# Optimization experiments

Hardware: AMD Instinct MI355X
Metric: run time of the kernel (lower is better)

The kernel has to match this reference:

```python
import jax, jax.numpy as jnp
import numpy as np

N_TOKENS = 2048
HIDDEN = 2880
N_HEADS = 64          # total query heads
N_KV = 8              # key/value heads
Q_MULT = N_HEADS // N_KV
HEAD_DIM = 64
SLIDING_WINDOW = 128  # layer_idx=0 -> sliding-window layer
SM_SCALE = 1.0 / np.sqrt(HEAD_DIM)
RMS_EPS = 1e-5
ROPE_BASE = 150000.0
ROPE_SCALING = 32.0
INIT_CTX = 4096
NTK_ALPHA = 1.0
NTK_BETA = 32.0


def _rope_tables(num_tokens):
    # YaRN NTK-by-parts inverse frequencies (static constants)
    freq = ROPE_BASE ** (np.arange(0, HEAD_DIM, 2, dtype=np.float64) / HEAD_DIM)
    concentration = 0.1 * np.log(ROPE_SCALING) + 1.0
    d_half = HEAD_DIM / 2
    low = d_half * np.log(INIT_CTX / (NTK_BETA * 2 * np.pi)) / np.log(ROPE_BASE)
    high = d_half * np.log(INIT_CTX / (NTK_ALPHA * 2 * np.pi)) / np.log(ROPE_BASE)
    interpolation = 1.0 / (ROPE_SCALING * freq)
    extrapolation = 1.0 / freq
    ramp = (np.arange(d_half) - low) / (high - low)
    m = 1.0 - np.clip(ramp, 0.0, 1.0)
    inv_freq = interpolation * (1.0 - m) + extrapolation * m
    t = np.arange(num_tokens, dtype=np.float64)
    freqs = np.outer(t, inv_freq)
    cos = jnp.asarray((np.cos(freqs) * concentration), dtype=jnp.float32)
    sin = jnp.asarray((np.sin(freqs) * concentration), dtype=jnp.float32)
    return cos, sin  # [num_tokens, HEAD_DIM//2]


def _apply_rotary(x, cos, sin):
    # x: [n, heads, HEAD_DIM]
    c = cos[:, None, :].astype(x.dtype)
    s = sin[:, None, :].astype(x.dtype)
    x1, x2 = jnp.split(x, 2, axis=-1)
    return jnp.concatenate([x1 * c - x2 * s, x2 * c + x1 * s], axis=-1)


def setup_inputs() -> dict:
    key = jax.random.key(0)
    ks = jax.random.split(key, 7)
    return {
        "x": jax.random.normal(ks[0], (N_TOKENS, HIDDEN), jnp.float32),
        "scale": jax.random.uniform(ks[1], (HIDDEN,), jnp.float32, 0.5, 1.5),
        "sink": jax.random.normal(ks[2], (N_HEADS,), jnp.float32),
        "w_qkv": jax.random.normal(ks[3], (HIDDEN, (N_HEADS + 2 * N_KV) * HEAD_DIM), jnp.float32) * 0.02,
        "b_qkv": jax.random.normal(ks[4], ((N_HEADS + 2 * N_KV) * HEAD_DIM,), jnp.float32) * 0.02,
        "w_o": jax.random.normal(ks[5], (N_HEADS * HEAD_DIM, HIDDEN), jnp.float32) * 0.02,
        "b_o": jax.random.normal(ks[6], (HIDDEN,), jnp.float32) * 0.02,
    }


def reference(x, scale, sink, w_qkv, b_qkv, w_o, b_o):
    n = x.shape[0]
    # RMSNorm (fp32)
    t = x.astype(jnp.float32)
    rms = jnp.sqrt(jnp.mean(t * t, axis=-1, keepdims=True) + RMS_EPS)
    t = (t / rms) * scale

    # QKV projection + split
    qkv = t @ w_qkv + b_qkv
    q_sz = N_HEADS * HEAD_DIM
    kv_sz = N_KV * HEAD_DIM
    q = qkv[:, :q_sz].reshape(n, N_HEADS, HEAD_DIM)
    k = qkv[:, q_sz:q_sz + kv_sz].reshape(n, N_KV, HEAD_DIM)
    v = qkv[:, q_sz + kv_sz:].reshape(n, N_KV, HEAD_DIM)

    # RoPE (YaRN)
    cos, sin = _rope_tables(n)
    q = _apply_rotary(q, cos, sin)
    k = _apply_rotary(k, cos, sin)

    # GQA layout: [n, N_KV, Q_MULT, HEAD_DIM]
    qg = q.reshape(n, N_KV, Q_MULT, HEAD_DIM)

    # scores: [N_KV, Q_MULT, n_q, n_kv]
    scores = jnp.einsum('nhgd,mhd->hgnm', qg, k) * SM_SCALE

    # causal + sliding-window mask
    q_pos = jnp.arange(n)[:, None]
    kv_pos = jnp.arange(n)[None, :]
    mask = jnp.where(kv_pos > q_pos, -jnp.inf, 0.0)
    mask = mask + jnp.where((SLIDING_WINDOW > 0) & (q_pos - kv_pos > SLIDING_WINDOW), -jnp.inf, 0.0)
    scores = scores + mask[None, None, :, :].astype(scores.dtype)

    # sink logit appended as extra softmax column, then dropped
    s_col = jnp.broadcast_to(sink.reshape(N_KV, Q_MULT, 1, 1), (N_KV, Q_MULT, n, 1))
    w = jax.nn.softmax(jnp.concatenate([scores, s_col], axis=-1), axis=-1)[..., :-1]

    attn = jnp.einsum('hgnm,mhd->nhgd', w, v).reshape(n, N_HEADS * HEAD_DIM)
    out = attn @ w_o + b_o
    return x + out


if __name__ == '__main__':
    inp = setup_inputs()
    y = reference(**inp)
    print(y.shape, y.dtype)
```

## Files before the change

### kernel.cpp

```cpp
#include <hip/hip_runtime.h>
#include <cstdint>
#include <cstddef>

#define HIDDEN   2880
#define QKV_N    5120
#define OPROJ_K  4096
#define NTOK     2048
#define WIN      128
#define SM_SCALE 0.125f

typedef _Float16 half8  __attribute__((ext_vector_type(8)));
typedef _Float16 half4v __attribute__((ext_vector_type(4)));
typedef float    f32x4  __attribute__((ext_vector_type(4)));

__device__ __forceinline__ void gload16(const void* g, void* l) {
  __builtin_amdgcn_global_load_lds((__attribute__((address_space(1))) void*)g,
                                   (__attribute__((address_space(3))) void*)l,
                                   16, 0, 0);
}

__device__ __forceinline__ _Float16 f2h(float f) { return (_Float16)f; }

#define NB_T0  (80 * 45)
#define NB_T1  (46 * 64)
#define NB_ROPE 256

__device__ __forceinline__ void cast_transpose64(const float* __restrict__ W,
                                                 _Float16* __restrict__ Wt,
                                                 int K, int N, int n0, int k0,
                                                 float* tile ) {
  int t = threadIdx.x;
  #pragma unroll
  for (int p = 0; p < 16; ++p) {
    int r = p * 4 + (t >> 6), cc = t & 63;
    float vv = 0.f;
    if (n0 + cc < N) vv = W[(size_t)(k0 + r) * N + n0 + cc];
    tile[r * 65 + cc] = vv;
  }
  __syncthreads();
  #pragma unroll
  for (int p = 0; p < 2; ++p) {
    int idx = p * 256 + t;
    int r = idx >> 3, ch = (idx & 7) * 8;
    half8 h;
    #pragma unroll
    for (int u = 0; u < 8; ++u) h[u] = (_Float16)tile[(ch + u) * 65 + r];
    *(half8*)&Wt[(size_t)(n0 + r) * K + k0 + ch] = h;
  }
}

__global__ __launch_bounds__(256) void prep_kernel(const float* __restrict__ x,
                                                   const float* __restrict__ scale,
                                                   const float* __restrict__ w_qkv,
                                                   const float* __restrict__ w_o,
                                                   _Float16* __restrict__ a_h,
                                                   _Float16* __restrict__ wtq,
                                                   _Float16* __restrict__ wto,
                                                   float2* __restrict__ tab) {
  __shared__ float smem[64 * 65];
  int b = blockIdx.x, t = threadIdx.x;
  if (b < NB_T0) {
    cast_transpose64(w_qkv, wtq, HIDDEN, QKV_N, (b % 80) * 64, (b / 80) * 64, smem);
    return;
  }
  b -= NB_T0;
  if (b < NB_T1) {
    cast_transpose64(w_o, wto, OPROJ_K, HIDDEN, (b % 46) * 64, (b / 46) * 64, smem);
    return;
  }
  b -= NB_T1;
  if (b < NTOK) {
    int row = b;
    const float4* xr = (const float4*)(x + (size_t)row * HIDDEN);
    const float4* sc = (const float4*)scale;
    float4 v0 = xr[t];
    float4 v1 = xr[t + 256];
    float4 v2 = (t < 208) ? xr[t + 512] : make_float4(0.f, 0.f, 0.f, 0.f);
    float ss = v0.x*v0.x + v0.y*v0.y + v0.z*v0.z + v0.w*v0.w
             + v1.x*v1.x + v1.y*v1.y + v1.z*v1.z + v1.w*v1.w
             + v2.x*v2.x + v2.y*v2.y + v2.z*v2.z + v2.w*v2.w;
    #pragma unroll
    for (int m = 1; m < 64; m <<= 1) ss += __shfl_xor(ss, m, 64);
    if ((t & 63) == 0) smem[t >> 6] = ss;
    __syncthreads();
    float inv = 1.0f / sqrtf((smem[0] + smem[1] + smem[2] + smem[3]) * (1.0f / HIDDEN) + 1e-5f);
    _Float16* orow = a_h + (size_t)row * HIDDEN;
    auto store4 = [&](int c4, const float4& v, const float4& s) {
      half4v h;
      h[0] = f2h(v.x * inv * s.x); h[1] = f2h(v.y * inv * s.y);
      h[2] = f2h(v.z * inv * s.z); h[3] = f2h(v.w * inv * s.w);
      *(half4v*)(orow + (size_t)c4 * 4) = h;
    };
    store4(t, v0, sc[t]);
    store4(t + 256, v1, sc[t + 256]);
    if (t < 208) store4(t + 512, v2, sc[t + 512]);
    return;
  }
  b -= NTOK;
  {
    int idx = b * 256 + t;
    int tok = idx >> 5, d = idx & 31;
    const double PI = 3.14159265358979323846;
    double i = (double)d;
    double lf = log(150000.0);
    double freq = exp(lf * (i / 32.0));
    double interp = 1.0 / (32.0 * freq);
    double extrap = 1.0 / freq;
    double low  = 32.0 * log(4096.0 / (32.0 * 2.0 * PI)) / lf;
    double high = 32.0 * log(4096.0 / (2.0 * PI)) / lf;
    double ramp = (i - low) / (high - low);
    double mm = 1.0 - fmin(fmax(ramp, 0.0), 1.0);
    double invf = interp * (1.0 - mm) + extrap * mm;
    double ang = (double)tok * invf;
    double conc = 0.1 * log(32.0) + 1.0;
    tab[idx] = make_float2((float)(cos(ang) * conc), (float)(sin(ang) * conc));
  }
}

#define QBM 128
#define QBN 320

__global__ __launch_bounds__(512, 2) void qkv8_kernel(const _Float16* __restrict__ A,
                                                      const _Float16* __restrict__ Bt,
                                                      const float* __restrict__ bias,
                                                      const float2* __restrict__ tab,
                                                      _Float16* __restrict__ out,
                                                      int K) {
  extern __shared__ char smem[];
  int tid = threadIdx.x;
  int wave = tid >> 6, lane = tid & 63;
  int wm = wave >> 2, wn = wave & 3;
  int c = lane & 15, quad = lane >> 4;
  int n0 = blockIdx.x * QBN, m0 = blockIdx.y * QBM;
  int NT = K >> 6;

  const _Float16* gA[2];
  #pragma unroll
  for (int i = 0; i < 2; ++i) {
    int ci = i * 512 + tid, r = ci >> 3, lc = (ci & 7) ^ (r & 7);
    gA[i] = A + (size_t)(m0 + r) * K + lc * 8;
  }
  const _Float16* gB[5];
  #pragma unroll
  for (int i = 0; i < 5; ++i) {
    int ci = i * 512 + tid, r = ci >> 3, lc = (ci & 7) ^ (r & 7);
    gB[i] = Bt + (size_t)(n0 + r) * K + lc * 8;
  }
  char* lA = smem + (size_t)(wave * 64) * 16;
  char* lB = smem + 32768 + (size_t)(wave * 64) * 16;

  auto STAGE = [&](int sel, int t) {
    size_t ko = (size_t)t * 64;
    #pragma unroll
    for (int i = 0; i < 2; ++i) gload16(gA[i] + ko, lA + sel * 16384 + i * 8192);
    #pragma unroll
    for (int i = 0; i < 5; ++i) gload16(gB[i] + ko, lB + sel * 40960 + i * 8192);
  };

  int aoff[2], boff[2];
  #pragma unroll
  for (int ks = 0; ks < 2; ++ks) {
    int px = ((ks * 4 + quad) ^ (c & 7)) * 16;
    aoff[ks] = (wm * 64 + c) * 128 + px;
    boff[ks] = (wn * 80 + c) * 128 + px;
  }

  f32x4 acc[4][5] = {};
  STAGE(0, 0);
  STAGE(1, 1);

  #pragma unroll 1
  for (int t = 0; t < NT; ++t) {
    if (t + 1 < NT) asm volatile("s_waitcnt vmcnt(7)" ::: "memory");
    else            asm volatile("s_waitcnt vmcnt(0)" ::: "memory");
    __builtin_amdgcn_s_barrier();
    asm volatile("" ::: "memory");
    const char* Ab = smem + (t & 1) * 16384;
    const char* Bb = smem + 32768 + (t & 1) * 40960;
    half8 a[4][2], b[5][2];
    #pragma unroll
    for (int i = 0; i < 4; ++i) {
      a[i][0] = *(const half8*)(Ab + aoff[0] + i * 2048);
      a[i][1] = *(const half8*)(Ab + aoff[1] + i * 2048);
    }
    #pragma unroll
    for (int j = 0; j < 5; ++j) {
      b[j][0] = *(const half8*)(Bb + boff[0] + j * 2048);
      b[j][1] = *(const half8*)(Bb + boff[1] + j * 2048);
    }
    __builtin_amdgcn_s_setprio(1);
    #pragma unroll
    for (int j = 0; j < 5; ++j)
      #pragma unroll
      for (int i = 0; i < 4; ++i)
        acc[i][j] = __builtin_amdgcn_mfma_f32_16x16x32_f16(a[i][0], b[j][0], acc[i][j], 0, 0, 0);
    __builtin_amdgcn_s_setprio(0);
    asm volatile("s_waitcnt lgkmcnt(0)" ::: "memory");
    __builtin_amdgcn_s_barrier();
    asm volatile("" ::: "memory");
    if (t + 2 < NT) STAGE(t & 1, t + 2);
    __builtin_amdgcn_s_setprio(1);
    #pragma unroll
    for (int j = 0; j < 5; ++j)
      #pragma unroll
      for (int i = 0; i < 4; ++i)
        acc[i][j] = __builtin_amdgcn_mfma_f32_16x16x32_f16(a[i][1], b[j][1], acc[i][j], 0, 0, 0);
    __builtin_amdgcn_s_setprio(0);
  }

  asm volatile("s_waitcnt lgkmcnt(0)" ::: "memory");
  __builtin_amdgcn_s_barrier();
  asm volatile("" ::: "memory");
  float* fP = (float*)smem;
  #pragma unroll
  for (int h = 0; h < 2; ++h) {
    if (wm == h) {
      #pragma unroll
      for (int j = 0; j < 5; ++j) {
        int coll = wn * 80 + j * 16 + c;
        float bv = bias[n0 + coll];
        #pragma unroll
        for (int i = 0; i < 4; ++i) {
          int rowl = i * 16 + quad * 4;
          #pragma unroll
          for (int r = 0; r < 4; ++r)
            fP[(rowl + r) * 324 + coll] = acc[i][j][r] + bv;
        }
      }
    }
    asm volatile("s_waitcnt lgkmcnt(0)" ::: "memory");
    __builtin_amdgcn_s_barrier();
    asm volatile("" ::: "memory");
    #pragma unroll
    for (int p = 0; p < 20; ++p) {
      int idx = p * 512 + tid;
      int row = idx / 160, s = idx - row * 160;
      int head = s >> 5, d = s & 31;
      int coll = head * 64 + d;
      int gcol = n0 + coll;
      int grow = m0 + h * 64 + row;
      float x1 = fP[row * 324 + coll];
      float x2 = fP[row * 324 + coll + 32];
      float2 cs = (gcol < 4608) ? tab[(size_t)grow * 32 + d] : make_float2(1.f, 0.f);
      out[(size_t)grow * QKV_N + gcol]      = f2h(x1 * cs.x - x2 * cs.y);
      out[(size_t)grow * QKV_N + gcol + 32] = f2h(x2 * cs.x + x1 * cs.y);
    }
    if (h == 0) {
      asm volatile("s_waitcnt lgkmcnt(0)" ::: "memory");
      __builtin_amdgcn_s_barrier();
      asm volatile("" ::: "memory");
    }
  }
}

template <int BM, bool QKV_MODE, int MINW>
__global__ __launch_bounds__(256, MINW) void gemm_kernel(const _Float16* __restrict__ A,
                                                         const _Float16* __restrict__ Bt,
                                                         const float* __restrict__ bias,
                                                         const float* __restrict__ resid,
                                                         const float2* __restrict__ tab,
                                                         void* __restrict__ Cout,
                                                         int M, int N, int K) {
  constexpr int MI = BM / 32;
  constexpr int NA = BM / 32;
  __shared__ _Float16 Alds[BM * 64];
  __shared__ _Float16 Blds[128 * 64];
  int tid = threadIdx.x;
  int wave = tid >> 6, lane = tid & 63;
  int wm = wave >> 1, wn = wave & 1;
  int c = lane & 15, quad = lane >> 4;
  int m0 = blockIdx.y * BM, n0 = blockIdx.x * 128;

  const _Float16* gAp[NA]; _Float16* lAp[NA];
  #pragma unroll
  for (int i = 0; i < NA; ++i) {
    int p = wave * 64 + i * 256 + lane;
    int r = p >> 3;
    int kl = (p & 7) ^ (r & 7);
    gAp[i] = A + (size_t)(m0 + r) * K + kl * 8;
    lAp[i] = Alds + (size_t)(wave * 64 + i * 256) * 8;
  }
  const _Float16* gBp[4]; _Float16* lBp[4];
  #pragma unroll
  for (int i = 0; i < 4; ++i) {
    int p = wave * 64 + i * 256 + lane;
    int r = p >> 3;
    int kl = (p & 7) ^ (r & 7);
    gBp[i] = Bt + (size_t)(n0 + r) * K + kl * 8;
    lBp[i] = Blds + (size_t)(wave * 64 + i * 256) * 8;
  }

  int px[2];
  px[0] = ((0 * 4 + quad) ^ (c & 7)) * 8;
  px[1] = ((1 * 4 + quad) ^ (c & 7)) * 8;

  f32x4 acc[MI][4] = {};
  int nIter = K >> 6;
  for (int kt = 0; kt < nIter; ++kt) {
    __syncthreads();
    #pragma unroll
    for (int i = 0; i < NA; ++i) { gload16(gAp[i], lAp[i]); gAp[i] += 64; }
    #pragma unroll
    for (int i = 0; i < 4; ++i)  { gload16(gBp[i], lBp[i]); gBp[i] += 64; }
    __syncthreads();
    half8 a[MI][2], b[4][2];
    #pragma unroll
    for (int i = 0; i < MI; ++i) {
      int row = wm * (BM / 2) + i * 16 + c;
      a[i][0] = *(const half8*)&Alds[row * 64 + px[0]];
      a[i][1] = *(const half8*)&Alds[row * 64 + px[1]];
    }
    #pragma unroll
    for (int j = 0; j < 4; ++j) {
      int row = wn * 64 + j * 16 + c;
      b[j][0] = *(const half8*)&Blds[row * 64 + px[0]];
      b[j][1] = *(const half8*)&Blds[row * 64 + px[1]];
    }
    #pragma unroll
    for (int i = 0; i < MI; ++i)
      #pragma unroll
      for (int j = 0; j < 4; ++j) {
        acc[i][j] = __builtin_amdgcn_mfma_f32_16x16x32_f16(a[i][0], b[j][0], acc[i][j], 0, 0, 0);
        acc[i][j] = __builtin_amdgcn_mfma_f32_16x16x32_f16(a[i][1], b[j][1], acc[i][j], 0, 0, 0);
      }
  }

  if (QKV_MODE) {
    _Float16* outp = (_Float16*)Cout;
    bool ropeTile = (n0 < 4608);
    #pragma unroll
    for (int i = 0; i < MI; ++i) {
      int rowb = m0 + wm * (BM / 2) + i * 16 + quad * 4;
      if (ropeTile) {
        #pragma unroll
        for (int jp = 0; jp < 2; ++jp) {
          int col = n0 + wn * 64 + jp * 16 + c;
          float b1 = bias[col], b2 = bias[col + 32];
          #pragma unroll
          for (int r = 0; r < 4; ++r) {
            float2 cs = tab[(size_t)(rowb + r) * 32 + jp * 16 + c];
            float x1 = acc[i][jp][r] + b1;
            float x2 = acc[i][jp + 2][r] + b2;
            outp[(size_t)(rowb + r) * QKV_N + col]      = f2h(x1 * cs.x - x2 * cs.y);
            outp[(size_t)(rowb + r) * QKV_N + col + 32] = f2h(x2 * cs.x + x1 * cs.y);
          }
        }
      } else {
        #pragma unroll
        for (int j = 0; j < 4; ++j) {
          int col = n0 + wn * 64 + j * 16 + c;
          float bv = bias[col];
          #pragma unroll
          for (int r = 0; r < 4; ++r)
            outp[(size_t)(rowb + r) * QKV_N + col] = f2h(acc[i][j][r] + bv);
        }
      }
    }
  } else {
    float* outp = (float*)Cout;
    #pragma unroll
    for (int i = 0; i < MI; ++i) {
      int rowb = m0 + wm * (BM / 2) + i * 16 + quad * 4;
      #pragma unroll
      for (int j = 0; j < 4; ++j) {
        int col = n0 + wn * 64 + j * 16 + c;
        if (col < N) {
          float bv = bias[col];
          #pragma unroll
          for (int r = 0; r < 4; ++r)
            outp[(size_t)(rowb + r) * N + col] =
                acc[i][j][r] + bv + resid[(size_t)(rowb + r) * N + col];
        }
      }
    }
  }
}

#define TQ 16
__global__ __launch_bounds__(256) void attn_kernel(const _Float16* __restrict__ qkv,
                                                   const float* __restrict__ sink,
                                                   _Float16* __restrict__ attn_out) {
  __shared__ __align__(16) char smem[61440];
  _Float16* Klds = (_Float16*)smem;
  _Float16* Qlds = (_Float16*)(smem + 20480);
  _Float16* Ps   = (_Float16*)smem;
  _Float16* Vt   = (_Float16*)(smem + 40960);

  int qt = blockIdx.x, kvh = blockIdx.y;
  int Q0 = qt * TQ;
  int kmin = (Q0 >= WIN) ? Q0 - WIN : 0;
  int nkv = Q0 + TQ - kmin;
  int tid = threadIdx.x;
  int wave = tid >> 6, lane = tid & 63;
  int c = lane & 15, quad = lane >> 4;

  {
    const _Float16* kbase = qkv + 4096 + kvh * 64;
    #pragma unroll
    for (int p = 0; p < 5; ++p) {
      int ci = p * 256 + wave * 64 + lane;
      int row = ci >> 3, pc = ci & 7;
      int lc = pc ^ (row & 7);
      gload16(kbase + (size_t)(kmin + row) * QKV_N + lc * 8,
              (char*)Klds + (size_t)(p * 256 + wave * 64) * 16);
    }
  }
  {
    const _Float16* qbase = qkv + kvh * 512;
    #pragma unroll
    for (int p = 0; p < 4; ++p) {
      int ci = p * 256 + wave * 64 + lane;
      int tok = ci >> 6, Lp = ci & 63;
      int Llog = (Lp & 56) | ((Lp ^ tok) & 7);
      gload16(qbase + (size_t)(Q0 + tok) * QKV_N + Llog * 8,
              (char*)Qlds + (size_t)(p * 256 + wave * 64) * 16);
    }
  }
  #pragma unroll
  for (int p = 0; p < 5; ++p) {
    int cc = p * 256 + tid;
    int col = cc % 160;
    int d0 = (cc / 160) * 8;
    union { uint4 u4; _Float16 hv[8]; } buf;
    if (col < nkv) buf.u4 = *(const uint4*)(qkv + (size_t)(kmin + col) * QKV_N + 4608 + kvh * 64 + d0);
    else           buf.u4 = make_uint4(0, 0, 0, 0);
    #pragma unroll
    for (int uu = 0; uu < 8; ++uu) Vt[(d0 + uu) * 160 + col] = buf.hv[uu];
  }

  __syncthreads();

  half8 aq[2][2];
  #pragma unroll
  for (int i = 0; i < 2; ++i) {
    int qm = wave * 2 + i;
    #pragma unroll
    for (int ks = 0; ks < 2; ++ks) {
      int kc = ks * 4 + quad;
      int Lp = qm * 8 + (kc ^ (c & 7));
      aq[i][ks] = *(const half8*)&Qlds[c * 512 + Lp * 8];
    }
  }

  f32x4 sacc[2][9] = {};
  #pragma unroll
  for (int j = 0; j < 9; ++j) {
    #pragma unroll
    for (int ks = 0; ks < 2; ++ks) {
      int kc = ks * 4 + quad;
      int pc = kc ^ (c & 7);
      half8 bk = *(const half8*)&Klds[(j * 16 + c) * 64 + pc * 8];
      #pragma unroll
      for (int i = 0; i < 2; ++i)
        sacc[i][j] = __builtin_amdgcn_mfma_f32_16x16x32_f16(aq[i][ks], bk, sacc[i][j], 0, 0, 0);
    }
  }

  __syncthreads();

  #pragma unroll
  for (int p = 0; p < 8; ++p) {
    int idx = p * 256 + tid;
    Ps[(idx >> 4) * 160 + 144 + (idx & 15)] = (_Float16)0.f;
  }

  #pragma unroll
  for (int i = 0; i < 2; ++i) {
    int qm = wave * 2 + i;
    float sk = sink[kvh * 8 + qm];
    #pragma unroll
    for (int r = 0; r < 4; ++r) {
      int qpos = Q0 + quad * 4 + r;
      float sv[9]; float mx = -3e38f;
      #pragma unroll
      for (int j = 0; j < 9; ++j) {
        int key = kmin + j * 16 + c;
        float s = sacc[i][j][r] * SM_SCALE;
        bool valid = (key <= qpos) && (qpos - key <= WIN);
        sv[j] = valid ? s : -3e38f;
        mx = fmaxf(mx, sv[j]);
      }
      #pragma unroll
      for (int msk = 1; msk < 16; msk <<= 1) mx = fmaxf(mx, __shfl_xor(mx, msk, 64));
      mx = fmaxf(mx, sk);
      float sum = 0.f; float pv[9];
      #pragma unroll
      for (int j = 0; j < 9; ++j) { float p = __expf(sv[j] - mx); pv[j] = p; sum += p; }
      #pragma unroll
      for (int msk = 1; msk < 16; msk <<= 1) sum += __shfl_xor(sum, msk, 64);
      sum += __expf(sk - mx);
      float inv = 1.0f / sum;
      int mrow = qm * 16 + quad * 4 + r;
      #pragma unroll
      for (int j = 0; j < 9; ++j)
        Ps[mrow * 160 + j * 16 + c] = f2h(pv[j] * inv);
    }
  }

  __syncthreads();

  f32x4 oacc[2][4] = {};
  #pragma unroll
  for (int ks = 0; ks < 5; ++ks) {
    half8 ap[2], bv[4];
    #pragma unroll
    for (int i = 0; i < 2; ++i)
      ap[i] = *(const half8*)&Ps[((wave * 2 + i) * 16 + c) * 160 + ks * 32 + quad * 8];
    #pragma unroll
    for (int j = 0; j < 4; ++j)
      bv[j] = *(const half8*)&Vt[(j * 16 + c) * 160 + ks * 32 + quad * 8];
    #pragma unroll
    for (int i = 0; i < 2; ++i)
      #pragma unroll
      for (int j = 0; j < 4; ++j)
        oacc[i][j] = __builtin_amdgcn_mfma_f32_16x16x32_f16(ap[i], bv[j], oacc[i][j], 0, 0, 0);
  }

  #pragma unroll
  for (int i = 0; i < 2; ++i) {
    int qm = wave * 2 + i;
    #pragma unroll
    for (int j = 0; j < 4; ++j)
      #pragma unroll
      for (int r = 0; r < 4; ++r) {
        int token = Q0 + quad * 4 + r;
        attn_out[(size_t)token * 4096 + (kvh * 8 + qm) * 64 + j * 16 + c] = f2h(oacc[i][j][r]);
      }
  }
}

extern "C" void kernel_launch(void* const* d_in, const int* in_sizes, int n_in,
                              void* d_out, int out_size, void* d_ws, size_t ws_size,
                              hipStream_t stream) {
  (void)in_sizes; (void)n_in; (void)out_size; (void)ws_size;
  const float* x      = (const float*)d_in[0];
  const float* scale  = (const float*)d_in[1];
  const float* sink   = (const float*)d_in[2];
  const float* w_qkv  = (const float*)d_in[3];
  const float* b_qkv  = (const float*)d_in[4];
  const float* w_o    = (const float*)d_in[5];
  const float* b_o    = (const float*)d_in[6];
  float* out = (float*)d_out;

  char* ws = (char*)d_ws;
  size_t off = 0;
  auto alloc = [&](size_t bytes) { void* p = ws + off; off += (bytes + 255) & ~(size_t)255; return p; };
  _Float16* wtq   = (_Float16*)alloc((size_t)QKV_N * HIDDEN * 2);
  _Float16* wto   = (_Float16*)alloc((size_t)2944 * OPROJ_K * 2);
  _Float16* a_h   = (_Float16*)alloc((size_t)NTOK * HIDDEN * 2);
  _Float16* qkv_h = (_Float16*)alloc((size_t)NTOK * QKV_N * 2);
  float2*   tab   = (float2*)alloc((size_t)NTOK * 32 * sizeof(float2));
  _Float16* at_h  = (_Float16*)wtq;

  static int qkv_attr_set = 0;
  if (!qkv_attr_set) {
    hipFuncSetAttribute((const void*)qkv8_kernel,
                        hipFuncAttributeMaxDynamicSharedMemorySize, 114688);
    qkv_attr_set = 1;
  }

  int prep_blocks = NB_T0 + NB_T1 + NTOK + NB_ROPE;
  prep_kernel<<<prep_blocks, 256, 0, stream>>>(x, scale, w_qkv, w_o, a_h, wtq, wto, tab);
  qkv8_kernel<<<dim3(QKV_N / QBN, NTOK / QBM), 512, 114688, stream>>>(
      a_h, wtq, b_qkv, tab, qkv_h, HIDDEN);
  attn_kernel<<<dim3(NTOK / TQ, 8), 256, 0, stream>>>(qkv_h, sink, at_h);
  gemm_kernel<64, false, 4><<<dim3(23, NTOK / 64), 256, 0, stream>>>(
      at_h, wto, b_o, x, nullptr, out, NTOK, HIDDEN, OPROJ_K);
}
```

Before: 338.3 us.

## Retile QKV GEMM to 256x256 with interleaved staging and direct RoPE epilogue

Changes the QKV projection tile from 128x320 to 256x256, giving each wave a 128x64 sub-tile with 32 accumulators. The K-loop is split into four quadrant phases, and the global-to-LDS loads for stage t+2 are spread between them to overlap with MFMA work. The epilogue now applies bias and RoPE straight from registers, pairing columns j and j+2 (offset 32), so the LDS transpose pass is gone. In exchange, LDS use grows to 128KB, which likely caps the kernel at one block per CU, and the grid shrinks to 160 blocks on a 256-CU part, so register pressure and occupancy become risks.

```diff
diff --git a/kernel.cpp b/kernel.cpp
--- a/kernel.cpp
+++ b/kernel.cpp
@@ -117,8 +117,8 @@
   }
 }
 
-#define QBM 128
-#define QBN 320
+#define QBM 256
+#define QBN 256
 
 __global__ __launch_bounds__(512, 2) void qkv8_kernel(const _Float16* __restrict__ A,
                                                       const _Float16* __restrict__ Bt,
@@ -134,121 +134,154 @@
   int n0 = blockIdx.x * QBN, m0 = blockIdx.y * QBM;
   int NT = K >> 6;
 
-  const _Float16* gA[2];
-  #pragma unroll
-  for (int i = 0; i < 2; ++i) {
+  const _Float16* gA[4];
+  const _Float16* gB[4];
+  #pragma unroll
+  for (int i = 0; i < 4; ++i) {
     int ci = i * 512 + tid, r = ci >> 3, lc = (ci & 7) ^ (r & 7);
     gA[i] = A + (size_t)(m0 + r) * K + lc * 8;
-  }
-  const _Float16* gB[5];
-  #pragma unroll
-  for (int i = 0; i < 5; ++i) {
-    int ci = i * 512 + tid, r = ci >> 3, lc = (ci & 7) ^ (r & 7);
     gB[i] = Bt + (size_t)(n0 + r) * K + lc * 8;
   }
   char* lA = smem + (size_t)(wave * 64) * 16;
-  char* lB = smem + 32768 + (size_t)(wave * 64) * 16;
-
-  auto STAGE = [&](int sel, int t) {
-    size_t ko = (size_t)t * 64;
-    #pragma unroll
-    for (int i = 0; i < 2; ++i) gload16(gA[i] + ko, lA + sel * 16384 + i * 8192);
-    #pragma unroll
-    for (int i = 0; i < 5; ++i) gload16(gB[i] + ko, lB + sel * 40960 + i * 8192);
+  char* lB = smem + 65536 + (size_t)(wave * 64) * 16;
+
+  auto stageA = [&](int sel, int t2, int i) {
+    gload16(gA[i] + (size_t)t2 * 64, lA + sel * 32768 + i * 8192);
   };
-
-  int aoff[2], boff[2];
-  #pragma unroll
-  for (int ks = 0; ks < 2; ++ks) {
-    int px = ((ks * 4 + quad) ^ (c & 7)) * 16;
-    aoff[ks] = (wm * 64 + c) * 128 + px;
-    boff[ks] = (wn * 80 + c) * 128 + px;
-  }
-
-  f32x4 acc[4][5] = {};
-  STAGE(0, 0);
-  STAGE(1, 1);
+  auto stageB = [&](int sel, int t2, int i) {
+    gload16(gB[i] + (size_t)t2 * 64, lB + sel * 32768 + i * 8192);
+  };
+
+  int px0 = ((0 * 4 + quad) ^ (c & 7)) * 16;
+  int px1 = ((1 * 4 + quad) ^ (c & 7)) * 16;
+  int arow = (wm * 128 + c) * 128;
+  int brow = (wn * 64 + c) * 128;
+
+  f32x4 acc[8][4] = {};
+
+  #pragma unroll
+  for (int i = 0; i < 4; ++i) { stageA(0, 0, i); stageB(0, 0, i); }
+  #pragma unroll
+  for (int i = 0; i < 4; ++i) { stageA(1, 1, i); stageB(1, 1, i); }
 
   #pragma unroll 1
   for (int t = 0; t < NT; ++t) {
-    if (t + 1 < NT) asm volatile("s_waitcnt vmcnt(7)" ::: "memory");
+    if (t + 1 < NT) asm volatile("s_waitcnt vmcnt(8)" ::: "memory");
     else            asm volatile("s_waitcnt vmcnt(0)" ::: "memory");
     __builtin_amdgcn_s_barrier();
     asm volatile("" ::: "memory");
-    const char* Ab = smem + (t & 1) * 16384;
-    const char* Bb = smem + 32768 + (t & 1) * 40960;
-    half8 a[4][2], b[5][2];
+    const char* Ab = smem + (t & 1) * 32768;
+    const char* Bb = smem + 65536 + (t & 1) * 32768;
+    int sel = t & 1;
+    int t2 = t + 2;
+    bool st = (t2 < NT);
+    half8 a[4][2], b[4][2];
+
     #pragma unroll
     for (int i = 0; i < 4; ++i) {
-      a[i][0] = *(const half8*)(Ab + aoff[0] + i * 2048);
-      a[i][1] = *(const half8*)(Ab + aoff[1] + i * 2048);
-    }
-    #pragma unroll
-    for (int j = 0; j < 5; ++j) {
-      b[j][0] = *(const half8*)(Bb + boff[0] + j * 2048);
-      b[j][1] = *(const half8*)(Bb + boff[1] + j * 2048);
-    }
+      a[i][0] = *(const half8*)(Ab + arow + i * 2048 + px0);
+      a[i][1] = *(const half8*)(Ab + arow + i * 2048 + px1);
+    }
+    #pragma unroll
+    for (int j = 0; j < 2; ++j) {
+      b[j][0] = *(const half8*)(Bb + brow + j * 2048 + px0);
+      b[j][1] = *(const half8*)(Bb + brow + j * 2048 + px1);
+    }
+    asm volatile("" ::: "memory");
+    __builtin_amdgcn_s_barrier();
+    asm volatile("s_waitcnt lgkmcnt(0)" ::: "memory");
     __builtin_amdgcn_s_setprio(1);
     #pragma unroll
-    for (int j = 0; j < 5; ++j)
-      #pragma unroll
-      for (int i = 0; i < 4; ++i)
+    for (int j = 0; j < 2; ++j)
+      #pragma unroll
+      for (int i = 0; i < 4; ++i) {
         acc[i][j] = __builtin_amdgcn_mfma_f32_16x16x32_f16(a[i][0], b[j][0], acc[i][j], 0, 0, 0);
+        acc[i][j] = __builtin_amdgcn_mfma_f32_16x16x32_f16(a[i][1], b[j][1], acc[i][j], 0, 0, 0);
+      }
     __builtin_amdgcn_s_setprio(0);
+    asm volatile("" ::: "memory");
+    __builtin_amdgcn_s_barrier();
+    asm volatile("" ::: "memory");
+
+    #pragma unroll
+    for (int j = 2; j < 4; ++j) {
+      b[j][0] = *(const half8*)(Bb + brow + j * 2048 + px0);
+      b[j][1] = *(const half8*)(Bb + brow + j * 2048 + px1);
+    }
+    if (st) { stageA(sel, t2, 0); stageA(sel, t2, 2); }
+    asm volatile("" ::: "memory");
+    __builtin_amdgcn_s_barrier();
     asm volatile("s_waitcnt lgkmcnt(0)" ::: "memory");
+    __builtin_amdgcn_s_setprio(1);
+    #pragma unroll
+    for (int j = 2; j < 4; ++j)
+      #pragma unroll
+      for (int i = 0; i < 4; ++i) {
+        acc[i][j] = __builtin_amdgcn_mfma_f32_16x16x32_f16(a[i][0], b[j][0], acc[i][j], 0, 0, 0);
+        acc[i][j] = __builtin_amdgcn_mfma_f32_16x16x32_f16(a[i][1], b[j][1], acc[i][j], 0, 0, 0);
+      }
+    __builtin_amdgcn_s_setprio(0);
+    asm volatile("" ::: "memory");
     __builtin_amdgcn_s_barrier();
     asm volatile("" ::: "memory");
-    if (t + 2 < NT) STAGE(t & 1, t + 2);
+
+    #pragma unroll
+    for (int i = 0; i < 4; ++i) {
+      a[i][0] = *(const half8*)(Ab + arow + (4 + i) * 2048 + px0);
+      a[i][1] = *(const half8*)(Ab + arow + (4 + i) * 2048 + px1);
+    }
+    if (st) { stageB(sel, t2, 0); stageB(sel, t2, 1); }
+    asm volatile("" ::: "memory");
+    __builtin_amdgcn_s_barrier();
+    asm volatile("s_waitcnt lgkmcnt(0)" ::: "memory");
     __builtin_amdgcn_s_setprio(1);
     #pragma unroll
-    for (int j = 0; j < 5; ++j)
-      #pragma unroll
-      for (int i = 0; i < 4; ++i)
-        acc[i][j] = __builtin_amdgcn_mfma_f32_16x16x32_f16(a[i][1], b[j][1], acc[i][j], 0, 0, 0);
+    for (int j = 2; j < 4; ++j)
+      #pragma unroll
+      for (int i = 0; i < 4; ++i) {
+        acc[4 + i][j] = __builtin_amdgcn_mfma_f32_16x16x32_f16(a[i][0], b[j][0], acc[4 + i][j], 0, 0, 0);
+        acc[4 + i][j] = __builtin_amdgcn_mfma_f32_16x16x32_f16(a[i][1], b[j][1], acc[4 + i][j], 0, 0, 0);
+      }
     __builtin_amdgcn_s_setprio(0);
-  }
-
-  asm volatile("s_waitcnt lgkmcnt(0)" ::: "memory");
-  __builtin_amdgcn_s_barrier();
-  asm volatile("" ::: "memory");
-  float* fP = (float*)smem;
-  #pragma unroll
-  for (int h = 0; h < 2; ++h) {
-    if (wm == h) {
-      #pragma unroll
-      for (int j = 0; j < 5; ++j) {
-        int coll = wn * 80 + j * 16 + c;
-        float bv = bias[n0 + coll];
-        #pragma unroll
-        for (int i = 0; i < 4; ++i) {
-          int rowl = i * 16 + quad * 4;
-          #pragma unroll
-          for (int r = 0; r < 4; ++r)
-            fP[(rowl + r) * 324 + coll] = acc[i][j][r] + bv;
+    asm volatile("" ::: "memory");
+    __builtin_amdgcn_s_barrier();
+    asm volatile("" ::: "memory");
+
+    if (st) { stageA(sel, t2, 1); stageA(sel, t2, 3); stageB(sel, t2, 2); stageB(sel, t2, 3); }
+    asm volatile("" ::: "memory");
+    __builtin_amdgcn_s_setprio(1);
+    #pragma unroll
+    for (int j = 0; j < 2; ++j)
+      #pragma unroll
+      for (int i = 0; i < 4; ++i) {
+        acc[4 + i][j] = __builtin_amdgcn_mfma_f32_16x16x32_f16(a[i][0], b[j][0], acc[4 + i][j], 0, 0, 0);
+        acc[4 + i][j] = __builtin_amdgcn_mfma_f32_16x16x32_f16(a[i][1], b[j][1], acc[4 + i][j], 0, 0, 0);
+      }
+    __builtin_amdgcn_s_setprio(0);
+    asm volatile("" ::: "memory");
+  }
+
+  bool rope = (n0 + wn * 64) < 4608;
+  #pragma unroll
+  for (int mi = 0; mi < 8; ++mi) {
+    int rowb = m0 + wm * 128 + mi * 16 + quad * 4;
+    #pragma unroll
+    for (int jp = 0; jp < 2; ++jp) {
+      int col = n0 + wn * 64 + jp * 16 + c;
+      float b1 = bias[col], b2 = bias[col + 32];
+      #pragma unroll
+      for (int r = 0; r < 4; ++r) {
+        float x1 = acc[mi][jp][r] + b1;
+        float x2 = acc[mi][jp + 2][r] + b2;
+        if (rope) {
+          float2 cs = tab[(size_t)(rowb + r) * 32 + jp * 16 + c];
+          out[(size_t)(rowb + r) * QKV_N + col]      = f2h(x1 * cs.x - x2 * cs.y);
+          out[(size_t)(rowb + r) * QKV_N + col + 32] = f2h(x2 * cs.x + x1 * cs.y);
+        } else {
+          out[(size_t)(rowb + r) * QKV_N + col]      = f2h(x1);
+          out[(size_t)(rowb + r) * QKV_N + col + 32] = f2h(x2);
         }
       }
-    }
-    asm volatile("s_waitcnt lgkmcnt(0)" ::: "memory");
-    __builtin_amdgcn_s_barrier();
-    asm volatile("" ::: "memory");
-    #pragma unroll
-    for (int p = 0; p < 20; ++p) {
-      int idx = p * 512 + tid;
-      int row = idx / 160, s = idx - row * 160;
-      int head = s >> 5, d = s & 31;
-      int coll = head * 64 + d;
-      int gcol = n0 + coll;
-      int grow = m0 + h * 64 + row;
-      float x1 = fP[row * 324 + coll];
-      float x2 = fP[row * 324 + coll + 32];
-      float2 cs = (gcol < 4608) ? tab[(size_t)grow * 32 + d] : make_float2(1.f, 0.f);
-      out[(size_t)grow * QKV_N + gcol]      = f2h(x1 * cs.x - x2 * cs.y);
-      out[(size_t)grow * QKV_N + gcol + 32] = f2h(x2 * cs.x + x1 * cs.y);
-    }
-    if (h == 0) {
-      asm volatile("s_waitcnt lgkmcnt(0)" ::: "memory");
-      __builtin_amdgcn_s_barrier();
-      asm volatile("" ::: "memory");
     }
   }
 }
@@ -555,13 +588,13 @@
   static int qkv_attr_set = 0;
   if (!qkv_attr_set) {
     hipFuncSetAttribute((const void*)qkv8_kernel,
-                        hipFuncAttributeMaxDynamicSharedMemorySize, 114688);
+                        hipFuncAttributeMaxDynamicSharedMemorySize, 131072);
     qkv_attr_set = 1;
   }
 
   int prep_blocks = NB_T0 + NB_T1 + NTOK + NB_ROPE;
   prep_kernel<<<prep_blocks, 256, 0, stream>>>(x, scale, w_qkv, w_o, a_h, wtq, wto, tab);
-  qkv8_kernel<<<dim3(QKV_N / QBN, NTOK / QBM), 512, 114688, stream>>>(
+  qkv8_kernel<<<dim3(QKV_N / QBN, NTOK / QBM), 512, 131072, stream>>>(
       a_h, wtq, b_qkv, tab, qkv_h, HIDDEN);
   attn_kernel<<<dim3(NTOK / TQ, 8), 256, 0, stream>>>(qkv_h, sink, at_h);
   gemm_kernel<64, false, 4><<<dim3(23, NTOK / 64), 256, 0, stream>>>(
```

Result: slower. 357.4 us (+5.7%).
